# Kernel tuning notes

Hardware: AMD Instinct MI355X
Metric: run time of the kernel (lower is better)

Reference implementation:

```python
import jax, jax.numpy as jnp
import numpy as np


def _compute_wavelet(scaling_rec):
    # g_k = h_{M-k-1}, with sign flip on odd indices (note: torch code flips
    # first, then negates odd indices of the flipped filter).
    g = jnp.flip(scaling_rec, axis=-1)
    signs = jnp.where(jnp.arange(g.shape[-1]) % 2 == 1, -1.0, 1.0).astype(g.dtype)
    return g * signs


def _convolve(x, filt):
    # Circular convolution via rFFT, matching torch.fft.rfft/irfft semantics.
    n = x.shape[-1]
    ra = jnp.fft.rfft(x)
    rb = jnp.fft.rfft(filt, n=n)
    return jnp.fft.irfft(ra * rb, n=n).astype(x.dtype)


def setup_inputs() -> dict:
    key = jax.random.key(0)
    k1, k2, k3 = jax.random.split(key, 3)
    inp = jax.random.normal(k1, (4096, 8192), dtype=jnp.float32)
    scaling = jax.random.normal(k2, (8,), dtype=jnp.float32)
    scaling_rec = jax.random.normal(k3, (8,), dtype=jnp.float32)
    return {"input": inp, "scaling": scaling, "scaling_rec": scaling_rec}


def reference(input, scaling, scaling_rec):
    wavelet = _compute_wavelet(scaling_rec)
    even = input[:, ::2]   # (n, m/2)
    odd = input[:, 1::2]   # (n, m/2)
    odd_updated = odd - _convolve(even, wavelet)
    even_updated = even - _convolve(odd, scaling)
    return (even_updated, odd_updated)
```

## Files before the change

### kernel.cpp

```cpp
#include <hip/hip_runtime.h>


#define COLS       8192
#define HALF       4096
#define PAIRS_PT   8
#define NTHREADS   256
#define THREADS_PER_ROW (HALF / PAIRS_PT)

__global__ __launch_bounds__(NTHREADS) void fwd_dwt_kernel(
    const float* __restrict__ input,
    const float* __restrict__ scaling,
    const float* __restrict__ scaling_rec,
    float* __restrict__ out,
    int rows)
{
    const int g     = blockIdx.x * NTHREADS + threadIdx.x;
    const int row   = g / THREADS_PER_ROW;
    const int chunk = g % THREADS_PER_ROW;
    const int k0    = chunk * PAIRS_PT;
    const int lane  = threadIdx.x & 63;

    const float* in_row = input + (size_t)row * COLS;

    float w[8], sc[8];
#pragma unroll
    for (int j = 0; j < 8; ++j) {
        w[j]  = scaling_rec[7 - j] * ((j & 1) ? -1.0f : 1.0f);
        sc[j] = scaling[j];
    }

    float4 v[4];
    const float4* p_pay = (const float4*)(in_row + 2 * k0);
#pragma unroll
    for (int i = 0; i < 4; ++i) v[i] = p_pay[i];

    float E[8], O[8];
#pragma unroll
    for (int i = 0; i < 4; ++i) {
        E[2 * i]     = v[i].x;  O[2 * i]     = v[i].y;
        E[2 * i + 1] = v[i].z;  O[2 * i + 1] = v[i].w;
    }

    float EF[15], OF[15];
#pragma unroll
    for (int i = 0; i < 8; ++i) { EF[7 + i] = E[i]; OF[7 + i] = O[i]; }
#pragma unroll
    for (int i = 1; i < 8; ++i) {
        EF[i - 1] = __shfl_up(E[i], 1);
        OF[i - 1] = __shfl_up(O[i], 1);
    }

    if (lane == 0) {
        const int hb = (k0 - PAIRS_PT) & (HALF - 1);
        const float4* p_halo = (const float4*)(in_row + 2 * hb);
        float4 h[4];
#pragma unroll
        for (int i = 0; i < 4; ++i) h[i] = p_halo[i];
#pragma unroll
        for (int p = 1; p < 8; ++p) {
            EF[p - 1] = (p & 1) ? h[p / 2].z : h[p / 2].x;
            OF[p - 1] = (p & 1) ? h[p / 2].w : h[p / 2].y;
        }
    }

    float eo[8], oo[8];
#pragma unroll
    for (int q = 0; q < 8; ++q) {
        float a = 0.0f, b = 0.0f;
#pragma unroll
        for (int j = 0; j < 8; ++j) {
            a += OF[7 + q - j] * sc[j];
            b += EF[7 + q - j] * w[j];
        }
        eo[q] = E[q] - a;
        oo[q] = O[q] - b;
    }

    float* oe = out + (size_t)row * HALF + k0;
    float* od = out + (size_t)rows * HALF + (size_t)row * HALF + k0;

    ((float4*)oe)[0] = make_float4(eo[0], eo[1], eo[2], eo[3]);
    ((float4*)oe)[1] = make_float4(eo[4], eo[5], eo[6], eo[7]);
    ((float4*)od)[0] = make_float4(oo[0], oo[1], oo[2], oo[3]);
    ((float4*)od)[1] = make_float4(oo[4], oo[5], oo[6], oo[7]);
}

extern "C" void kernel_launch(void* const* d_in, const int* in_sizes, int n_in,
                              void* d_out, int out_size, void* d_ws, size_t ws_size,
                              hipStream_t stream) {
    const float* input       = (const float*)d_in[0];
    const float* scaling     = (const float*)d_in[1];
    const float* scaling_rec = (const float*)d_in[2];
    float*       out         = (float*)d_out;

    const int rows    = in_sizes[0] / COLS;
    const int threads = rows * THREADS_PER_ROW;
    fwd_dwt_kernel<<<threads / NTHREADS, NTHREADS, 0, stream>>>(
        input, scaling, scaling_rec, out, rows);
}
```

Baseline: 233.2 us.

## Grid-stride four chunks per thread with software-prefetched next loads

Each thread now handles four chunks in a grid-stride loop. It issues the global loads for the next chunk before computing the current one, so memory latency overlaps the FIR arithmetic. The grid shrinks fourfold, launch bounds ask for occupancy 4, and filter coefficients are loaded once per thread. The cost is higher register pressure from double-buffered data and fewer waves to hide latency on a bandwidth-bound kernel.

```diff
diff --git a/kernel.cpp b/kernel.cpp
--- a/kernel.cpp
+++ b/kernel.cpp
@@ -5,22 +5,19 @@
 #define HALF       4096
 #define PAIRS_PT   8
 #define NTHREADS   256
-#define THREADS_PER_ROW (HALF / PAIRS_PT)
+#define CHUNKS_PER_ROW (HALF / PAIRS_PT)
+#define ITERS      4
 
-__global__ __launch_bounds__(NTHREADS) void fwd_dwt_kernel(
+__global__ __launch_bounds__(NTHREADS, 4) void fwd_dwt_kernel(
     const float* __restrict__ input,
     const float* __restrict__ scaling,
     const float* __restrict__ scaling_rec,
     float* __restrict__ out,
     int rows)
 {
-    const int g     = blockIdx.x * NTHREADS + threadIdx.x;
-    const int row   = g / THREADS_PER_ROW;
-    const int chunk = g % THREADS_PER_ROW;
-    const int k0    = chunk * PAIRS_PT;
-    const int lane  = threadIdx.x & 63;
-
-    const float* in_row = input + (size_t)row * COLS;
+    const int lane   = threadIdx.x & 63;
+    const int stride = gridDim.x * NTHREADS;
+    int c = blockIdx.x * NTHREADS + threadIdx.x;
 
     float w[8], sc[8];
 #pragma unroll
@@ -29,60 +26,88 @@
         sc[j] = scaling[j];
     }
 
-    float4 v[4];
-    const float4* p_pay = (const float4*)(in_row + 2 * k0);
+    float4 v[4], h[4];
+
+    {
+        const float* in_row = input + (size_t)(c >> 9) * COLS;
+        const int k0 = (c & (CHUNKS_PER_ROW - 1)) * PAIRS_PT;
+        const float4* p = (const float4*)(in_row + 2 * k0);
 #pragma unroll
-    for (int i = 0; i < 4; ++i) v[i] = p_pay[i];
-
-    float E[8], O[8];
+        for (int i = 0; i < 4; ++i) v[i] = p[i];
+        if (lane == 0) {
+            const int hb = (k0 - PAIRS_PT) & (HALF - 1);
+            const float4* ph = (const float4*)(in_row + 2 * hb);
 #pragma unroll
-    for (int i = 0; i < 4; ++i) {
-        E[2 * i]     = v[i].x;  O[2 * i]     = v[i].y;
-        E[2 * i + 1] = v[i].z;  O[2 * i + 1] = v[i].w;
-    }
-
-    float EF[15], OF[15];
-#pragma unroll
-    for (int i = 0; i < 8; ++i) { EF[7 + i] = E[i]; OF[7 + i] = O[i]; }
-#pragma unroll
-    for (int i = 1; i < 8; ++i) {
-        EF[i - 1] = __shfl_up(E[i], 1);
-        OF[i - 1] = __shfl_up(O[i], 1);
-    }
-
-    if (lane == 0) {
-        const int hb = (k0 - PAIRS_PT) & (HALF - 1);
-        const float4* p_halo = (const float4*)(in_row + 2 * hb);
-        float4 h[4];
-#pragma unroll
-        for (int i = 0; i < 4; ++i) h[i] = p_halo[i];
-#pragma unroll
-        for (int p = 1; p < 8; ++p) {
-            EF[p - 1] = (p & 1) ? h[p / 2].z : h[p / 2].x;
-            OF[p - 1] = (p & 1) ? h[p / 2].w : h[p / 2].y;
+            for (int i = 0; i < 4; ++i) h[i] = ph[i];
         }
     }
 
-    float eo[8], oo[8];
 #pragma unroll
-    for (int q = 0; q < 8; ++q) {
-        float a = 0.0f, b = 0.0f;
+    for (int it = 0; it < ITERS; ++it) {
+        const int row = c >> 9;
+        const int k0  = (c & (CHUNKS_PER_ROW - 1)) * PAIRS_PT;
+
+        float E[8], O[8];
 #pragma unroll
-        for (int j = 0; j < 8; ++j) {
-            a += OF[7 + q - j] * sc[j];
-            b += EF[7 + q - j] * w[j];
+        for (int i = 0; i < 4; ++i) {
+            E[2 * i]     = v[i].x;  O[2 * i]     = v[i].y;
+            E[2 * i + 1] = v[i].z;  O[2 * i + 1] = v[i].w;
         }
-        eo[q] = E[q] - a;
-        oo[q] = O[q] - b;
+
+        float EF[15], OF[15];
+#pragma unroll
+        for (int i = 0; i < 8; ++i) { EF[7 + i] = E[i]; OF[7 + i] = O[i]; }
+#pragma unroll
+        for (int i = 1; i < 8; ++i) {
+            EF[i - 1] = __shfl_up(E[i], 1);
+            OF[i - 1] = __shfl_up(O[i], 1);
+        }
+        if (lane == 0) {
+#pragma unroll
+            for (int p = 1; p < 8; ++p) {
+                EF[p - 1] = (p & 1) ? h[p / 2].z : h[p / 2].x;
+                OF[p - 1] = (p & 1) ? h[p / 2].w : h[p / 2].y;
+            }
+        }
+
+        const int cn = c + stride;
+        if (it + 1 < ITERS) {
+            const float* in_rowN = input + (size_t)(cn >> 9) * COLS;
+            const int k0n = (cn & (CHUNKS_PER_ROW - 1)) * PAIRS_PT;
+            const float4* pn = (const float4*)(in_rowN + 2 * k0n);
+#pragma unroll
+            for (int i = 0; i < 4; ++i) v[i] = pn[i];
+            if (lane == 0) {
+                const int hbn = (k0n - PAIRS_PT) & (HALF - 1);
+                const float4* phn = (const float4*)(in_rowN + 2 * hbn);
+#pragma unroll
+                for (int i = 0; i < 4; ++i) h[i] = phn[i];
+            }
+        }
+
+        float eo[8], oo[8];
+#pragma unroll
+        for (int q = 0; q < 8; ++q) {
+            float a = 0.0f, b = 0.0f;
+#pragma unroll
+            for (int j = 0; j < 8; ++j) {
+                a += OF[7 + q - j] * sc[j];
+                b += EF[7 + q - j] * w[j];
+            }
+            eo[q] = E[q] - a;
+            oo[q] = O[q] - b;
+        }
+
+        float* oe = out + (size_t)row * HALF + k0;
+        float* od = out + (size_t)rows * HALF + (size_t)row * HALF + k0;
+
+        ((float4*)oe)[0] = make_float4(eo[0], eo[1], eo[2], eo[3]);
+        ((float4*)oe)[1] = make_float4(eo[4], eo[5], eo[6], eo[7]);
+        ((float4*)od)[0] = make_float4(oo[0], oo[1], oo[2], oo[3]);
+        ((float4*)od)[1] = make_float4(oo[4], oo[5], oo[6], oo[7]);
+
+        c = cn;
     }
-
-    float* oe = out + (size_t)row * HALF + k0;
-    float* od = out + (size_t)rows * HALF + (size_t)row * HALF + k0;
-
-    ((float4*)oe)[0] = make_float4(eo[0], eo[1], eo[2], eo[3]);
-    ((float4*)oe)[1] = make_float4(eo[4], eo[5], eo[6], eo[7]);
-    ((float4*)od)[0] = make_float4(oo[0], oo[1], oo[2], oo[3]);
-    ((float4*)od)[1] = make_float4(oo[4], oo[5], oo[6], oo[7]);
 }
 
 extern "C" void kernel_launch(void* const* d_in, const int* in_sizes, int n_in,
@@ -93,8 +118,9 @@
     const float* scaling_rec = (const float*)d_in[2];
     float*       out         = (float*)d_out;
 
-    const int rows    = in_sizes[0] / COLS;
-    const int threads = rows * THREADS_PER_ROW;
-    fwd_dwt_kernel<<<threads / NTHREADS, NTHREADS, 0, stream>>>(
+    const int rows   = in_sizes[0] / COLS;
+    const int chunks = rows * CHUNKS_PER_ROW;
+    const int blocks = chunks / (NTHREADS * ITERS);
+    fwd_dwt_kernel<<<blocks, NTHREADS, 0, stream>>>(
         input, scaling, scaling_rec, out, rows);
 }
```

Result: no change. 235.8 us (+1.1%).

## Assign one float4 per thread and gather halo via multi-distance shuffles

Applied to the files above, without the earlier changes.

Each thread now handles 2 output pairs from a single float4 load instead of 8 pairs from four float4 loads. This quadruples the thread count and yields perfectly coalesced 16-byte loads and 8-byte stores. The 7-tap history comes from shuffles at distances 1 to 4 with lane-dependent halo reloads. The extra shuffles per output and the narrower stores add instruction overhead in a kernel that is bandwidth-bound.

```diff
diff --git a/kernel.cpp b/kernel.cpp
--- a/kernel.cpp
+++ b/kernel.cpp
@@ -3,9 +3,8 @@
 
 #define COLS       8192
 #define HALF       4096
-#define PAIRS_PT   8
+#define F4_PER_ROW 2048
 #define NTHREADS   256
-#define THREADS_PER_ROW (HALF / PAIRS_PT)
 
 __global__ __launch_bounds__(NTHREADS) void fwd_dwt_kernel(
     const float* __restrict__ input,
@@ -14,11 +13,10 @@
     float* __restrict__ out,
     int rows)
 {
-    const int g     = blockIdx.x * NTHREADS + threadIdx.x;
-    const int row   = g / THREADS_PER_ROW;
-    const int chunk = g % THREADS_PER_ROW;
-    const int k0    = chunk * PAIRS_PT;
-    const int lane  = threadIdx.x & 63;
+    const int t    = blockIdx.x * NTHREADS + threadIdx.x;
+    const int row  = t >> 11;
+    const int tl   = t & (F4_PER_ROW - 1);
+    const int lane = threadIdx.x & 63;
 
     const float* in_row = input + (size_t)row * COLS;
 
@@ -29,60 +27,45 @@
         sc[j] = scaling[j];
     }
 
-    float4 v[4];
-    const float4* p_pay = (const float4*)(in_row + 2 * k0);
+    const float4 v = ((const float4*)in_row)[tl];
+
+    float u1x = __shfl_up(v.x, 1), u1y = __shfl_up(v.y, 1);
+    float u1z = __shfl_up(v.z, 1), u1w = __shfl_up(v.w, 1);
+    float u2x = __shfl_up(v.x, 2), u2y = __shfl_up(v.y, 2);
+    float u2z = __shfl_up(v.z, 2), u2w = __shfl_up(v.w, 2);
+    float u3x = __shfl_up(v.x, 3), u3y = __shfl_up(v.y, 3);
+    float u3z = __shfl_up(v.z, 3), u3w = __shfl_up(v.w, 3);
+    float u4z = __shfl_up(v.z, 4), u4w = __shfl_up(v.w, 4);
+
+    if (lane < 1) { const float4 h = ((const float4*)in_row)[(tl - 1) & (F4_PER_ROW - 1)];
+                    u1x = h.x; u1y = h.y; u1z = h.z; u1w = h.w; }
+    if (lane < 2) { const float4 h = ((const float4*)in_row)[(tl - 2) & (F4_PER_ROW - 1)];
+                    u2x = h.x; u2y = h.y; u2z = h.z; u2w = h.w; }
+    if (lane < 3) { const float4 h = ((const float4*)in_row)[(tl - 3) & (F4_PER_ROW - 1)];
+                    u3x = h.x; u3y = h.y; u3z = h.z; u3w = h.w; }
+    if (lane < 4) { const float4 h = ((const float4*)in_row)[(tl - 4) & (F4_PER_ROW - 1)];
+                    u4z = h.z; u4w = h.w; }
+
+    float pe[9], po[9];
+    pe[0] = u4z; po[0] = u4w;
+    pe[1] = u3x; po[1] = u3y;  pe[2] = u3z; po[2] = u3w;
+    pe[3] = u2x; po[3] = u2y;  pe[4] = u2z; po[4] = u2w;
+    pe[5] = u1x; po[5] = u1y;  pe[6] = u1z; po[6] = u1w;
+    pe[7] = v.x; po[7] = v.y;  pe[8] = v.z; po[8] = v.w;
+
+    float eo0 = pe[7], oo0 = po[7], eo1 = pe[8], oo1 = po[8];
 #pragma unroll
-    for (int i = 0; i < 4; ++i) v[i] = p_pay[i];
-
-    float E[8], O[8];
-#pragma unroll
-    for (int i = 0; i < 4; ++i) {
-        E[2 * i]     = v[i].x;  O[2 * i]     = v[i].y;
-        E[2 * i + 1] = v[i].z;  O[2 * i + 1] = v[i].w;
+    for (int j = 0; j < 8; ++j) {
+        eo0 -= po[7 - j] * sc[j];
+        oo0 -= pe[7 - j] * w[j];
+        eo1 -= po[8 - j] * sc[j];
+        oo1 -= pe[8 - j] * w[j];
     }
 
-    float EF[15], OF[15];
-#pragma unroll
-    for (int i = 0; i < 8; ++i) { EF[7 + i] = E[i]; OF[7 + i] = O[i]; }
-#pragma unroll
-    for (int i = 1; i < 8; ++i) {
-        EF[i - 1] = __shfl_up(E[i], 1);
-        OF[i - 1] = __shfl_up(O[i], 1);
-    }
-
-    if (lane == 0) {
-        const int hb = (k0 - PAIRS_PT) & (HALF - 1);
-        const float4* p_halo = (const float4*)(in_row + 2 * hb);
-        float4 h[4];
-#pragma unroll
-        for (int i = 0; i < 4; ++i) h[i] = p_halo[i];
-#pragma unroll
-        for (int p = 1; p < 8; ++p) {
-            EF[p - 1] = (p & 1) ? h[p / 2].z : h[p / 2].x;
-            OF[p - 1] = (p & 1) ? h[p / 2].w : h[p / 2].y;
-        }
-    }
-
-    float eo[8], oo[8];
-#pragma unroll
-    for (int q = 0; q < 8; ++q) {
-        float a = 0.0f, b = 0.0f;
-#pragma unroll
-        for (int j = 0; j < 8; ++j) {
-            a += OF[7 + q - j] * sc[j];
-            b += EF[7 + q - j] * w[j];
-        }
-        eo[q] = E[q] - a;
-        oo[q] = O[q] - b;
-    }
-
-    float* oe = out + (size_t)row * HALF + k0;
-    float* od = out + (size_t)rows * HALF + (size_t)row * HALF + k0;
-
-    ((float4*)oe)[0] = make_float4(eo[0], eo[1], eo[2], eo[3]);
-    ((float4*)oe)[1] = make_float4(eo[4], eo[5], eo[6], eo[7]);
-    ((float4*)od)[0] = make_float4(oo[0], oo[1], oo[2], oo[3]);
-    ((float4*)od)[1] = make_float4(oo[4], oo[5], oo[6], oo[7]);
+    float* oe = out + (size_t)row * HALF + 2 * tl;
+    float* od = out + (size_t)rows * HALF + (size_t)row * HALF + 2 * tl;
+    ((float2*)oe)[0] = make_float2(eo0, eo1);
+    ((float2*)od)[0] = make_float2(oo0, oo1);
 }
 
 extern "C" void kernel_launch(void* const* d_in, const int* in_sizes, int n_in,
@@ -94,7 +77,7 @@
     float*       out         = (float*)d_out;
 
     const int rows    = in_sizes[0] / COLS;
-    const int threads = rows * THREADS_PER_ROW;
+    const int threads = rows * F4_PER_ROW;
     fwd_dwt_kernel<<<threads / NTHREADS, NTHREADS, 0, stream>>>(
         input, scaling, scaling_rec, out, rows);
 }
```

After: 238.6 us. +2.3%, slower.
